# Optimization experiments

Measured on AMD Instinct MI355X. Metric: run time of the kernel, lower is better.

The kernel has to match this reference:

```python
import jax, jax.numpy as jnp
import numpy as np

# Problem dims (match init_kwargs)
N, D, H, W = 32, 64, 56, 56      # Xshape
F, P = 128, 4                    # n_filters, number_of_points
KH = 3                           # h_filter == w_filter
PAD = KH // 2                    # padw
ALPHA = 0.1                      # threshold sharpness for sigmoid approximation


def setup_inputs() -> dict:
    key = jax.random.key(0)
    k1, k2, k3 = jax.random.split(key, 3)
    return {
        "input": jax.random.normal(k1, (N, D, H, W), dtype=jnp.float32),
        # integer kernel coordinates in [0, KH): (filter, point, [ky, kx])
        "kernels": jax.random.randint(k2, (F, P, 2), 0, KH, dtype=jnp.int32),
        # channel projection indices in [0, D): (filter, point)
        "projection_map": jax.random.randint(k3, (F, P), 0, D, dtype=jnp.int32),
    }


def _lbp_forward(x, kernels, projection_map):
    # Pad spatially by PAD (zero padding), as the CUDA kernel pads input.
    xp = jnp.pad(x, ((0, 0), (0, 0), (PAD, PAD), (PAD, PAD)))  # [N, D, H+2P, W+2P]

    # Per (filter, point): gather the HxW window at integer offset (ky, kx)
    # from channel c of the padded input. vmap of dynamic_slice -> one fused gather.
    def sample(c, ky, kx):
        return jax.lax.dynamic_slice(xp, (0, c, ky, kx), (N, 1, H, W))[:, 0]  # [N,H,W]

    samp = jax.vmap(jax.vmap(sample))(
        projection_map, kernels[..., 0], kernels[..., 1]
    )  # [F, P, N, H, W]
    samp = jnp.transpose(samp, (2, 0, 1, 3, 4))  # [N, F, P, H, W]

    # Center pixel (same channel as the sampled point).
    center = xp[:, :, PAD:PAD + H, PAD:PAD + W]       # [N, D, H, W]
    cen = center[:, projection_map]                    # [N, F, P, H, W]

    # Output0: per-point sampled difference; threshold approximated by a
    # steep sigmoid (scale 1/ALPHA) so the op is differentiable, then pool
    # the P bits into a binary code with weights 2^p.
    diff = samp - cen                                  # [N, F, P, H, W]
    bits = jax.nn.sigmoid(diff / ALPHA)
    weights = jnp.asarray(2.0 ** np.arange(P), dtype=jnp.float32)  # [P]
    return jnp.einsum('nfphw,p->nfhw', bits, weights)  # [N, F, H, W]


def reference(input, kernels, projection_map):
    return _lbp_forward(input, kernels, projection_map)
```

## Files before the change

### kernel.cpp

```cpp
#include <hip/hip_runtime.h>


#define NN 32
#define DD 64
#define HH 56
#define WW 56
#define FF 128
#define PP 4

#define ROWS 7
#define TR   (ROWS + 2)
#define TC   64
#define COL0 4
#define CHS  (TR * TC)
#define TILE_FLOATS (DD * CHS)
#define NTHREADS 1024
#define NWAVES 16
#define FITER (FF / NWAVES)
#define ITEMS (DD * TR * (WW/4))
#define SCALE -14.4269504089f

__global__ __launch_bounds__(NTHREADS, 4) void lbp_kernel(
    const float* __restrict__ x,
    const int*   __restrict__ kern,
    const int*   __restrict__ proj,
    float*       __restrict__ out)
{
    __shared__ float tile[TILE_FLOATS];

    const int tid = threadIdx.x;
    const int n   = blockIdx.y;
    const int h0  = blockIdx.x * ROWS;

    for (int i = tid; i < DD * TR * 2; i += NTHREADS) {
        const int ch   = i / (TR * 2);
        const int rr   = (i >> 1) % TR;
        const int side = i & 1;
        tile[ch * CHS + rr * TC + 3 + side * 57] = 0.f;
    }

    const float* xn = x + (size_t)n * (DD * HH * WW);
    float4 rv[8];
    int    lo[8];
#pragma unroll
    for (int it = 0; it < 8; ++it) {
        const int item = tid + it * NTHREADS;
        rv[it] = make_float4(0.f, 0.f, 0.f, 0.f);
        lo[it] = -1;
        if (item < ITEMS) {
            const int ch  = item / (TR * 14);
            const int rem = item - ch * (TR * 14);
            const int tr  = rem / 14;
            const int v   = rem - tr * 14;
            lo[it] = ch * CHS + tr * TC + COL0 + 4 * v;
            const int h = h0 + tr - 1;
            if ((unsigned)h < (unsigned)HH)
                rv[it] = *(const float4*)(xn + ch * (HH * WW) + h * WW + 4 * v);
        }
    }
#pragma unroll
    for (int it = 0; it < 8; ++it) {
        if (lo[it] >= 0) {
            float4 v = rv[it];
            v.x *= SCALE; v.y *= SCALE; v.z *= SCALE; v.w *= SCALE;
            *(float4*)(tile + lo[it]) = v;
        }
    }
    __syncthreads();

    const int wid  = __builtin_amdgcn_readfirstlane(tid >> 6);
    const int lane = tid & 63;
    const int w    = lane < WW ? lane : WW - 1;
    const bool act = lane < WW;
    const int cb   = TC + COL0 + w;

    int f = wid;
    int4 pj = *(const int4*)(proj + f * PP);
    int4 ka = *(const int4*)(kern + f * (PP * 2));
    int4 kb = *(const int4*)(kern + f * (PP * 2) + 4);

#pragma unroll
    for (int k = 0; k < FITER; ++k) {
        const int fn = f + NWAVES;
        int4 pjn, kan, kbn;
        if (fn < FF) {
            pjn = *(const int4*)(proj + fn * PP);
            kan = *(const int4*)(kern + fn * (PP * 2));
            kbn = *(const int4*)(kern + fn * (PP * 2) + 4);
        }
        const int cc[4]  = {pj.x, pj.y, pj.z, pj.w};
        const int kyv[4] = {ka.x, ka.z, kb.x, kb.z};
        const int kxv[4] = {ka.y, ka.w, kb.y, kb.w};

        float acc[ROWS];
#pragma unroll
        for (int r = 0; r < ROWS; ++r) acc[r] = 0.f;

        float wt = 1.f;
#pragma unroll
        for (int p = 0; p < PP; ++p) {
            const int pc = cc[p] * CHS + cb;
            const int pn = pc + (kyv[p] - 1) * TC + (kxv[p] - 1);
#pragma unroll
            for (int r = 0; r < ROWS; ++r) {
                const float xv = tile[pc + r * TC];
                const float yv = tile[pn + r * TC];
                const float e  = __builtin_amdgcn_exp2f(yv - xv);
                acc[r] = fmaf(wt, __builtin_amdgcn_rcpf(1.f + e), acc[r]);
            }
            wt *= 2.f;
        }
        if (act) {
            float* op = out + ((size_t)n * FF + f) * (HH * WW)
                            + (size_t)h0 * WW + w;
#pragma unroll
            for (int r = 0; r < ROWS; ++r) op[r * WW] = acc[r];
        }
        f = fn; pj = pjn; ka = kan; kb = kbn;
    }
}

extern "C" void kernel_launch(void* const* d_in, const int* in_sizes, int n_in,
                              void* d_out, int out_size, void* d_ws, size_t ws_size,
                              hipStream_t stream) {
    const float* x    = (const float*)d_in[0];
    const int*   kern = (const int*)d_in[1];
    const int*   proj = (const int*)d_in[2];
    float*       out  = (float*)d_out;

    dim3 grid(HH / ROWS, NN);
    dim3 block(NTHREADS);
    lbp_kernel<<<grid, block, 0, stream>>>(x, kern, proj, out);
}
```

Before: 27.23 us.

## Split tile load into two row halves and use piecewise-linear sigmoid

Splits the shared-memory tile fill into two phases: the first five padded rows are stored and the first three output rows computed while the remaining rows' global loads are still in flight, then the rest are stored and computed. It also replaces the exp2/rcp sigmoid with a min of three linear pieces clamped at 0.4914, applied with the sign of the difference and added to a 7.5 offset. This drops the pre-scaling of the input. The aim is to hide global load latency behind compute and cut transcendental cost. The risks are extra register pressure from holding nine float4 loads, and a sigmoid that is only approximate and may not meet tolerance.

New measurement: 26.91 us. About the same (-1.2%).

```diff
diff --git a/kernel.cpp b/kernel.cpp
--- a/kernel.cpp
+++ b/kernel.cpp
@@ -17,8 +17,20 @@
 #define NTHREADS 1024
 #define NWAVES 16
 #define FITER (FF / NWAVES)
-#define ITEMS (DD * TR * (WW/4))
-#define SCALE -14.4269504089f
+
+#define ROWS_A 5
+#define ROWS_B 4
+#define ITEMS_A (DD * ROWS_A * 14)
+#define ITEMS_B (DD * ROWS_B * 14)
+
+#define SIG_ACC(d_, accv_, wt_) do {                                  \
+    const float ad_ = __builtin_fabsf(d_);                            \
+    const float u0_ = fmaf(2.5f,     ad_, -0.0078f);                  \
+    const float u1_ = fmaf(1.49146f, ad_,  0.08455f);                 \
+    const float u2_ = fmaf(0.45177f, ad_,  0.30774f);                 \
+    const float um_ = fminf(fminf(u0_, u1_), fminf(u2_, 0.49140f));   \
+    accv_ = fmaf(wt_, copysignf(um_, d_), accv_);                     \
+} while (0)
 
 __global__ __launch_bounds__(NTHREADS, 4) void lbp_kernel(
     const float* __restrict__ x,
@@ -32,6 +44,39 @@
     const int n   = blockIdx.y;
     const int h0  = blockIdx.x * ROWS;
 
+    const float* xn = x + (size_t)n * (DD * HH * WW);
+
+    float4 rv[9];
+    int    lo[9];
+#pragma unroll
+    for (int it = 0; it < 9; ++it) {
+        rv[it] = make_float4(0.f, 0.f, 0.f, 0.f);
+        lo[it] = -1;
+        int ch = -1, tr = 0, v = 0;
+        if (it < 5) {
+            const int item = tid + it * NTHREADS;
+            if (item < ITEMS_A) {
+                ch = item / (ROWS_A * 14);
+                const int rem = item - ch * (ROWS_A * 14);
+                tr = rem / 14; v = rem - tr * 14;
+            }
+        } else {
+            const int item = tid + (it - 5) * NTHREADS;
+            if (item < ITEMS_B) {
+                ch = item / (ROWS_B * 14);
+                const int rem = item - ch * (ROWS_B * 14);
+                const int t2 = rem / 14;
+                tr = ROWS_A + t2; v = rem - t2 * 14;
+            }
+        }
+        if (ch >= 0) {
+            lo[it] = ch * CHS + tr * TC + COL0 + 4 * v;
+            const int h = h0 + tr - 1;
+            if ((unsigned)h < (unsigned)HH)
+                rv[it] = *(const float4*)(xn + ch * (HH * WW) + h * WW + 4 * v);
+        }
+    }
+
     for (int i = tid; i < DD * TR * 2; i += NTHREADS) {
         const int ch   = i / (TR * 2);
         const int rr   = (i >> 1) % TR;
@@ -39,33 +84,9 @@
         tile[ch * CHS + rr * TC + 3 + side * 57] = 0.f;
     }
 
-    const float* xn = x + (size_t)n * (DD * HH * WW);
-    float4 rv[8];
-    int    lo[8];
 #pragma unroll
-    for (int it = 0; it < 8; ++it) {
-        const int item = tid + it * NTHREADS;
-        rv[it] = make_float4(0.f, 0.f, 0.f, 0.f);
-        lo[it] = -1;
-        if (item < ITEMS) {
-            const int ch  = item / (TR * 14);
-            const int rem = item - ch * (TR * 14);
-            const int tr  = rem / 14;
-            const int v   = rem - tr * 14;
-            lo[it] = ch * CHS + tr * TC + COL0 + 4 * v;
-            const int h = h0 + tr - 1;
-            if ((unsigned)h < (unsigned)HH)
-                rv[it] = *(const float4*)(xn + ch * (HH * WW) + h * WW + 4 * v);
-        }
-    }
-#pragma unroll
-    for (int it = 0; it < 8; ++it) {
-        if (lo[it] >= 0) {
-            float4 v = rv[it];
-            v.x *= SCALE; v.y *= SCALE; v.z *= SCALE; v.w *= SCALE;
-            *(float4*)(tile + lo[it]) = v;
-        }
-    }
+    for (int it = 0; it < 5; ++it)
+        if (lo[it] >= 0) *(float4*)(tile + lo[it]) = rv[it];
     __syncthreads();
 
     const int wid  = __builtin_amdgcn_readfirstlane(tid >> 6);
@@ -74,50 +95,61 @@
     const bool act = lane < WW;
     const int cb   = TC + COL0 + w;
 
-    int f = wid;
-    int4 pj = *(const int4*)(proj + f * PP);
-    int4 ka = *(const int4*)(kern + f * (PP * 2));
-    int4 kb = *(const int4*)(kern + f * (PP * 2) + 4);
+#define COMPUTE_HALF(R0, NR)                                              \
+  {                                                                       \
+    int f = wid;                                                          \
+    int4 pj = *(const int4*)(proj + f * PP);                              \
+    int4 ka = *(const int4*)(kern + f * (PP * 2));                        \
+    int4 kb = *(const int4*)(kern + f * (PP * 2) + 4);                    \
+    _Pragma("unroll")                                                     \
+    for (int k = 0; k < FITER; ++k) {                                     \
+      const int fn = f + NWAVES;                                          \
+      int4 pjn, kan, kbn;                                                 \
+      if (fn < FF) {                                                      \
+        pjn = *(const int4*)(proj + fn * PP);                             \
+        kan = *(const int4*)(kern + fn * (PP * 2));                       \
+        kbn = *(const int4*)(kern + fn * (PP * 2) + 4);                   \
+      }                                                                   \
+      const int cc[4]  = {pj.x, pj.y, pj.z, pj.w};                        \
+      const int kyv[4] = {ka.x, ka.z, kb.x, kb.z};                        \
+      const int kxv[4] = {ka.y, ka.w, kb.y, kb.w};                        \
+      float acc[NR];                                                      \
+      _Pragma("unroll")                                                   \
+      for (int r = 0; r < NR; ++r) acc[r] = 7.5f;         \
+      float wt = 1.f;                                                     \
+      _Pragma("unroll")                                                   \
+      for (int p = 0; p < PP; ++p) {                                      \
+        const int pc = cc[p] * CHS + cb + (R0) * TC;                      \
+        const int pn = pc + (kyv[p] - 1) * TC + (kxv[p] - 1);             \
+        _Pragma("unroll")                                                 \
+        for (int r = 0; r < NR; ++r) {                                    \
+          const float xv = tile[pc + r * TC];                             \
+          const float yv = tile[pn + r * TC];                             \
+          const float d_ = yv - xv;                                       \
+          SIG_ACC(d_, acc[r], wt);                                        \
+        }                                                                 \
+        wt *= 2.f;                                                        \
+      }                                                                   \
+      if (act) {                                                          \
+        float* op = out + ((size_t)n * FF + f) * (HH * WW)                \
+                        + (size_t)h0 * WW + w;                            \
+        _Pragma("unroll")                                                 \
+        for (int r = 0; r < NR; ++r) op[((R0) + r) * WW] = acc[r];        \
+      }                                                                   \
+      f = fn; pj = pjn; ka = kan; kb = kbn;                               \
+    }                                                                     \
+  }
+
+    COMPUTE_HALF(0, 3)
 
 #pragma unroll
-    for (int k = 0; k < FITER; ++k) {
-        const int fn = f + NWAVES;
-        int4 pjn, kan, kbn;
-        if (fn < FF) {
-            pjn = *(const int4*)(proj + fn * PP);
-            kan = *(const int4*)(kern + fn * (PP * 2));
-            kbn = *(const int4*)(kern + fn * (PP * 2) + 4);
-        }
-        const int cc[4]  = {pj.x, pj.y, pj.z, pj.w};
-        const int kyv[4] = {ka.x, ka.z, kb.x, kb.z};
-        const int kxv[4] = {ka.y, ka.w, kb.y, kb.w};
+    for (int it = 5; it < 9; ++it)
+        if (lo[it] >= 0) *(float4*)(tile + lo[it]) = rv[it];
+    __syncthreads();
 
-        float acc[ROWS];
-#pragma unroll
-        for (int r = 0; r < ROWS; ++r) acc[r] = 0.f;
+    COMPUTE_HALF(3, 4)
 
-        float wt = 1.f;
-#pragma unroll
-        for (int p = 0; p < PP; ++p) {
-            const int pc = cc[p] * CHS + cb;
-            const int pn = pc + (kyv[p] - 1) * TC + (kxv[p] - 1);
-#pragma unroll
-            for (int r = 0; r < ROWS; ++r) {
-                const float xv = tile[pc + r * TC];
-                const float yv = tile[pn + r * TC];
-                const float e  = __builtin_amdgcn_exp2f(yv - xv);
-                acc[r] = fmaf(wt, __builtin_amdgcn_rcpf(1.f + e), acc[r]);
-            }
-            wt *= 2.f;
-        }
-        if (act) {
-            float* op = out + ((size_t)n * FF + f) * (HH * WW)
-                            + (size_t)h0 * WW + w;
-#pragma unroll
-            for (int r = 0; r < ROWS; ++r) op[r * WW] = acc[r];
-        }
-        f = fn; pj = pjn; ka = kan; kb = kbn;
-    }
+#undef COMPUTE_HALF
 }
 
 extern "C" void kernel_launch(void* const* d_in, const int* in_sizes, int n_in,
```

## Store shared tile as packed fp16 row pairs and use packed half subtraction

Applied to the files above, without the earlier changes.

The shared-memory tile now holds the pre-scaled input as fp16, with two vertically adjacent rows packed into each 32-bit word. The compute loop loads four packed words per point for the center and four for the neighbor, re-aligns them for odd row offsets, and subtracts with packed half2 ops before converting back to fp32 for the sigmoid. This halves LDS footprint and the number of LDS reads per filter point. The cost is reduced precision in the scaled difference, which is amplified by the steep sigmoid and may cause accuracy drift, plus extra conversion and alignment ALU work.

Measured after the change: 29.82 us. 1.1x slower.

```diff
diff --git a/kernel.cpp b/kernel.cpp
--- a/kernel.cpp
+++ b/kernel.cpp
@@ -1,4 +1,5 @@
 #include <hip/hip_runtime.h>
+#include <hip/hip_fp16.h>
 
 
 #define NN 32
@@ -9,16 +10,29 @@
 #define PP 4
 
 #define ROWS 7
-#define TR   (ROWS + 2)
-#define TC   64
+#define NRP  5
+#define TCC  64
 #define COL0 4
-#define CHS  (TR * TC)
-#define TILE_FLOATS (DD * CHS)
+#define CHDW (NRP * TCC)
+#define TILE_DW (DD * CHDW)
 #define NTHREADS 1024
 #define NWAVES 16
 #define FITER (FF / NWAVES)
-#define ITEMS (DD * TR * (WW/4))
+#define NITEMS (DD * NRP * 14)
 #define SCALE -14.4269504089f
+
+__device__ __forceinline__ uint32_t ph_sub(uint32_t a, uint32_t b) {
+    __half2 ha = *(__half2*)&a, hb = *(__half2*)&b;
+    __half2 r  = __hsub2(ha, hb);
+    return *(uint32_t*)&r;
+}
+__device__ __forceinline__ uint32_t alignb(uint32_t hi, uint32_t lo) {
+    return (uint32_t)((((uint64_t)hi << 32) | lo) >> 16);
+}
+__device__ __forceinline__ float2 cvt2(uint32_t d) {
+    __half2 h = *(__half2*)&d;
+    return __half22float2(h);
+}
 
 __global__ __launch_bounds__(NTHREADS, 4) void lbp_kernel(
     const float* __restrict__ x,
@@ -26,44 +40,55 @@
     const int*   __restrict__ proj,
     float*       __restrict__ out)
 {
-    __shared__ float tile[TILE_FLOATS];
+    __shared__ uint32_t tile32[TILE_DW];
 
     const int tid = threadIdx.x;
     const int n   = blockIdx.y;
     const int h0  = blockIdx.x * ROWS;
 
-    for (int i = tid; i < DD * TR * 2; i += NTHREADS) {
-        const int ch   = i / (TR * 2);
-        const int rr   = (i >> 1) % TR;
-        const int side = i & 1;
-        tile[ch * CHS + rr * TC + 3 + side * 57] = 0.f;
+    const float* xn = x + (size_t)n * (DD * HH * WW);
+
+    float4 av[5], bv[5];
+    int    dst[5];
+#pragma unroll
+    for (int it = 0; it < 5; ++it) {
+        const int item = tid + it * NTHREADS;
+        av[it] = make_float4(0.f, 0.f, 0.f, 0.f);
+        bv[it] = make_float4(0.f, 0.f, 0.f, 0.f);
+        dst[it] = -1;
+        if (item < NITEMS) {
+            const int ch  = item / (NRP * 14);
+            const int rem = item - ch * (NRP * 14);
+            const int rp  = rem / 14;
+            const int vg  = rem - rp * 14;
+            dst[it] = (ch * NRP + rp) * TCC + COL0 + 4 * vg;
+            const int h0r = h0 + 2 * rp - 1;
+            const float* gp = xn + ch * (HH * WW) + 4 * vg;
+            if ((unsigned)h0r < (unsigned)HH)
+                av[it] = *(const float4*)(gp + h0r * WW);
+            if ((unsigned)(h0r + 1) < (unsigned)HH)
+                bv[it] = *(const float4*)(gp + (h0r + 1) * WW);
+        }
     }
 
-    const float* xn = x + (size_t)n * (DD * HH * WW);
-    float4 rv[8];
-    int    lo[8];
+    if (tid < DD * NRP * 2) {
+        const int side = tid & 1;
+        const int cr   = tid >> 1;
+        tile32[cr * TCC + 3 + side * 57] = 0u;
+    }
+
 #pragma unroll
-    for (int it = 0; it < 8; ++it) {
-        const int item = tid + it * NTHREADS;
-        rv[it] = make_float4(0.f, 0.f, 0.f, 0.f);
-        lo[it] = -1;
-        if (item < ITEMS) {
-            const int ch  = item / (TR * 14);
-            const int rem = item - ch * (TR * 14);
-            const int tr  = rem / 14;
-            const int v   = rem - tr * 14;
-            lo[it] = ch * CHS + tr * TC + COL0 + 4 * v;
-            const int h = h0 + tr - 1;
-            if ((unsigned)h < (unsigned)HH)
-                rv[it] = *(const float4*)(xn + ch * (HH * WW) + h * WW + 4 * v);
-        }
-    }
-#pragma unroll
-    for (int it = 0; it < 8; ++it) {
-        if (lo[it] >= 0) {
-            float4 v = rv[it];
-            v.x *= SCALE; v.y *= SCALE; v.z *= SCALE; v.w *= SCALE;
-            *(float4*)(tile + lo[it]) = v;
+    for (int it = 0; it < 5; ++it) {
+        if (dst[it] >= 0) {
+            uint32_t q[4];
+            const float4 a = av[it], b = bv[it];
+            __half2 h0p = __floats2half2_rn(SCALE * a.x, SCALE * b.x);
+            __half2 h1p = __floats2half2_rn(SCALE * a.y, SCALE * b.y);
+            __half2 h2p = __floats2half2_rn(SCALE * a.z, SCALE * b.z);
+            __half2 h3p = __floats2half2_rn(SCALE * a.w, SCALE * b.w);
+            q[0] = *(uint32_t*)&h0p; q[1] = *(uint32_t*)&h1p;
+            q[2] = *(uint32_t*)&h2p; q[3] = *(uint32_t*)&h3p;
+            *(uint4*)&tile32[dst[it]] = make_uint4(q[0], q[1], q[2], q[3]);
         }
     }
     __syncthreads();
@@ -72,12 +97,17 @@
     const int lane = tid & 63;
     const int w    = lane < WW ? lane : WW - 1;
     const bool act = lane < WW;
-    const int cb   = TC + COL0 + w;
+    const int wcol = COL0 + w;
 
     int f = wid;
     int4 pj = *(const int4*)(proj + f * PP);
     int4 ka = *(const int4*)(kern + f * (PP * 2));
     int4 kb = *(const int4*)(kern + f * (PP * 2) + 4);
+
+#define ACC1(vz, ar) do {                                         \
+    const float e_ = __builtin_amdgcn_exp2f(vz);                  \
+    ar = fmaf(wt, __builtin_amdgcn_rcpf(1.f + e_), ar);           \
+} while (0)
 
 #pragma unroll
     for (int k = 0; k < FITER; ++k) {
@@ -99,15 +129,37 @@
         float wt = 1.f;
 #pragma unroll
         for (int p = 0; p < PP; ++p) {
-            const int pc = cc[p] * CHS + cb;
-            const int pn = pc + (kyv[p] - 1) * TC + (kxv[p] - 1);
-#pragma unroll
-            for (int r = 0; r < ROWS; ++r) {
-                const float xv = tile[pc + r * TC];
-                const float yv = tile[pn + r * TC];
-                const float e  = __builtin_amdgcn_exp2f(yv - xv);
-                acc[r] = fmaf(wt, __builtin_amdgcn_rcpf(1.f + e), acc[r]);
+            const int ky   = kyv[p];
+            const int base = cc[p] * CHDW + wcol;
+            const int na   = base + (kxv[p] - 1) + ((ky == 2) ? TCC : 0);
+
+            const uint32_t c0 = tile32[base];
+            const uint32_t c1 = tile32[base + 64];
+            const uint32_t c2 = tile32[base + 128];
+            const uint32_t c3 = tile32[base + 192];
+            const uint32_t n0 = tile32[na];
+            const uint32_t n1 = tile32[na + 64];
+            const uint32_t n2 = tile32[na + 128];
+            const uint32_t n3 = tile32[na + 192];
+
+            uint32_t d0, d1, d2, d3;
+            if (ky == 1) {
+                d0 = ph_sub(n0, c0); d1 = ph_sub(n1, c1);
+                d2 = ph_sub(n2, c2); d3 = ph_sub(n3, c3);
+            } else {
+                const uint32_t s0 = alignb(n0, n0);
+                const uint32_t s1 = alignb(n1, n0);
+                const uint32_t s2 = alignb(n2, n1);
+                const uint32_t s3 = alignb(n3, n2);
+                d0 = ph_sub(s0, c0); d1 = ph_sub(s1, c1);
+                d2 = ph_sub(s2, c2); d3 = ph_sub(s3, c3);
             }
+            const float2 f0 = cvt2(d0), f1 = cvt2(d1);
+            const float2 f2 = cvt2(d2), f3 = cvt2(d3);
+            ACC1(f0.y, acc[0]);
+            ACC1(f1.x, acc[1]); ACC1(f1.y, acc[2]);
+            ACC1(f2.x, acc[3]); ACC1(f2.y, acc[4]);
+            ACC1(f3.x, acc[5]); ACC1(f3.y, acc[6]);
             wt *= 2.f;
         }
         if (act) {
@@ -118,6 +170,7 @@
         }
         f = fn; pj = pjn; ka = kan; kb = kbn;
     }
+#undef ACC1
 }
 
 extern "C" void kernel_launch(void* const* d_in, const int* in_sizes, int n_in,
```
